# Kernel optimization log

Measured on AMD Instinct MI355X. Metric: run time of the kernel, lower is better.

Reference implementation:

```python
import jax, jax.numpy as jnp
import numpy as np

NUM_HEADS = 16
HEAD_DIM = 64
D_MODEL = NUM_HEADS * HEAD_DIM


def setup_inputs() -> dict:
    key = jax.random.key(0)
    k1, k2, k3 = jax.random.split(key, 3)
    N, T = 2, 2048
    x = jax.random.normal(k1, (N, T, D_MODEL), dtype=jnp.float32)
    mask = jnp.ones((N, T), dtype=jnp.float32)
    # fused QKV projection params (Dense: H*D*3 outputs)
    W_qkv = jax.random.normal(k2, (D_MODEL, D_MODEL * 3), dtype=jnp.float32) * (D_MODEL ** -0.5)
    b_qkv = jnp.zeros((D_MODEL * 3,), dtype=jnp.float32)
    return {"x": x, "mask": mask, "W_qkv": W_qkv, "b_qkv": b_qkv}


def reference(x, mask, W_qkv, b_qkv):
    N, T, _ = x.shape
    H, D = NUM_HEADS, HEAD_DIM
    qkv = x @ W_qkv + b_qkv                       # [N, T, H*D*3]
    qkv = qkv.reshape(N, T, H, D, 3)
    qkv = jnp.transpose(qkv, (4, 0, 2, 1, 3))     # [3, N, H, T, D]
    q, k, v = qkv[0], qkv[1], qkv[2]
    logits = jnp.einsum('bhqd,bhkd->bhqk', q, k) / (D ** 0.5)  # [N, H, T, T]
    # NOTE: original masks along the QUERY axis (broadcast over keys)
    logits = logits + (1.0 - mask)[:, None, :, None] * -1e9
    w = jax.nn.softmax(logits, axis=-1)
    out = jnp.einsum('bhqk,bhkd->bhqd', w, v)     # [N, H, T, D]
    out = jnp.transpose(out, (0, 2, 1, 3)).reshape(N, T, H * D)
    return out
```

## Files before the change

kernel.cpp:

```cpp
#include <hip/hip_runtime.h>
#include <hip/hip_bf16.h>
#include <stdint.h>

#define NHEADS 16
#define HDIM   64
#define DMODEL 1024
#define SEQ    2048
#define NB     2
#define MTOT   (NB*SEQ)
#define NTOT   (3*DMODEL)
#define KTOT   DMODEL

#define QSCALE 0.18033688011112042f

typedef __attribute__((ext_vector_type(8)))  short          bf16x8;
typedef __attribute__((ext_vector_type(4)))  float          f32x4;
typedef __attribute__((ext_vector_type(8)))  unsigned short u16x8;

__device__ __forceinline__ unsigned short f2bf(float f) {
  unsigned u = __builtin_bit_cast(unsigned, f);
  u += 0x7fffu + ((u >> 16) & 1u);
  return (unsigned short)(u >> 16);
}

__device__ __forceinline__ f32x4 vmax4(f32x4 a, f32x4 b) {
  f32x4 r;
  r[0]=fmaxf(a[0],b[0]); r[1]=fmaxf(a[1],b[1]);
  r[2]=fmaxf(a[2],b[2]); r[3]=fmaxf(a[3],b[3]);
  return r;
}

__device__ __forceinline__ void async_copy16(void* lds, const void* g) {
  __builtin_amdgcn_global_load_lds(
      (const __attribute__((address_space(1))) unsigned int*)g,
      (__attribute__((address_space(3))) unsigned int*)lds, 16, 0, 0);
}

__global__ void convert_x_kernel(const float* __restrict__ x,
                                 unsigned short* __restrict__ xb) {
  int i = blockIdx.x * 256 + threadIdx.x;
  const f32x4* xv = reinterpret_cast<const f32x4*>(x);
  f32x4 a = xv[2*i];
  f32x4 b = xv[2*i + 1];
  u16x8 r;
  r[0]=f2bf(a[0]); r[1]=f2bf(a[1]); r[2]=f2bf(a[2]); r[3]=f2bf(a[3]);
  r[4]=f2bf(b[0]); r[5]=f2bf(b[1]); r[6]=f2bf(b[2]); r[7]=f2bf(b[3]);
  reinterpret_cast<u16x8*>(xb)[i] = r;
}

__global__ void transpose_w_kernel(const float* __restrict__ W,
                                   unsigned short* __restrict__ Wt) {
  __shared__ float tile[64][65];
  int j0 = blockIdx.x * 64;
  int k0 = blockIdx.y * 64;
  int tid = threadIdx.x;
  int lr = tid >> 6;
  int lc = tid & 63;
  #pragma unroll
  for (int i = 0; i < 16; ++i) {
    int r = i*4 + lr;
    tile[r][lc] = W[(size_t)(k0 + r)*NTOT + j0 + lc];
  }
  __syncthreads();
  #pragma unroll
  for (int i = 0; i < 16; ++i) {
    int jr = i*4 + lr;
    int j  = j0 + jr;
    int oc = (j % 3)*DMODEL + (j / 3);
    Wt[(size_t)oc*KTOT + k0 + lc] = f2bf(tile[lc][jr]);
  }
}

#define BM 128
#define BN 128
#define BK2 32
#define NBX (NTOT/BN)
#define NBY (MTOT/BM)
#define EPSTRIDE 136
__launch_bounds__(256)
__global__ void qkv_gemm_kernel(const unsigned short* __restrict__ xb,
                                const unsigned short* __restrict__ wt,
                                const float* __restrict__ bqkv,
                                unsigned short* __restrict__ Qb,
                                unsigned short* __restrict__ Kb,
                                unsigned short* __restrict__ Vt) {
  __shared__ __align__(16) unsigned char gsm[128*EPSTRIDE*2];
  unsigned short* As = (unsigned short*)gsm;
  unsigned short* Bs = (unsigned short*)(gsm + 16384);
  unsigned short* Ep = (unsigned short*)gsm;

  int tid = threadIdx.x;
  int w = tid >> 6, l = tid & 63;
  int m0 = blockIdx.y * BM;
  int n0 = blockIdx.x * BN;
  int ln = l & 15, lg = l >> 4;
  int wm = (w >> 1) * 64;
  int wn = (w & 1) * 64;

  f32x4 acc[4][4];
  const f32x4 zero4 = {0.f, 0.f, 0.f, 0.f};
  #pragma unroll
  for (int i = 0; i < 4; ++i)
    #pragma unroll
    for (int j = 0; j < 4; ++j) acc[i][j] = zero4;

  #define STAGE2(BUF, KT)                                                     \
  do {                                                                        \
    _Pragma("unroll")                                                         \
    for (int i = 0; i < 2; ++i) {                                             \
      int row  = i*64 + w*16 + (l >> 2);                                      \
      int seg  = (l & 3) ^ ((row >> 1) & 3);                                  \
      async_copy16(gsm + (BUF)*8192 + i*4096 + w*1024,                        \
                   &xb[(size_t)(m0 + row)*KTOT + (KT)*BK2 + seg*8]);          \
      async_copy16(gsm + 16384 + (BUF)*8192 + i*4096 + w*1024,                \
                   &wt[(size_t)(n0 + row)*KTOT + (KT)*BK2 + seg*8]);          \
    }                                                                         \
  } while (0)

  STAGE2(0, 0);
  asm volatile("s_waitcnt vmcnt(0)" ::: "memory");
  __syncthreads();

  for (int kt = 0; kt < KTOT/BK2; ++kt) {
    int cur = kt & 1;
    if (kt < KTOT/BK2 - 1) STAGE2(cur ^ 1, kt + 1);

    bf16x8 af[4], bfr[4];
    #pragma unroll
    for (int mi = 0; mi < 4; ++mi) {
      int ra = wm + mi*16 + ln;
      af[mi] = *reinterpret_cast<const bf16x8*>(
          &As[cur*4096 + ra*BK2 + ((lg ^ ((ra >> 1) & 3)) << 3)]);
    }
    #pragma unroll
    for (int ni = 0; ni < 4; ++ni) {
      int rb = wn + ni*16 + ln;
      bfr[ni] = *reinterpret_cast<const bf16x8*>(
          &Bs[cur*4096 + rb*BK2 + ((lg ^ ((rb >> 1) & 3)) << 3)]);
    }
    #pragma unroll
    for (int mi = 0; mi < 4; ++mi)
      #pragma unroll
      for (int ni = 0; ni < 4; ++ni)
        acc[mi][ni] = __builtin_amdgcn_mfma_f32_16x16x32_bf16(af[mi], bfr[ni], acc[mi][ni], 0, 0, 0);

    __syncthreads();
  }
  #undef STAGE2

  int r4 = lg * 4;
  if (n0 >= 2*DMODEL) {
    int hd0 = n0 - 2*DMODEL;
    #pragma unroll
    for (int mi = 0; mi < 4; ++mi) {
      #pragma unroll
      for (int ni = 0; ni < 4; ++ni) {
        int col = wn + ni*16 + ln;
        float bias = bqkv[(hd0 + col)*3 + 2];
        int rb = wm + mi*16 + r4;
        ushort4 pk4;
        pk4.x = f2bf(acc[mi][ni][0] + bias);
        pk4.y = f2bf(acc[mi][ni][1] + bias);
        pk4.z = f2bf(acc[mi][ni][2] + bias);
        pk4.w = f2bf(acc[mi][ni][3] + bias);
        *reinterpret_cast<ushort4*>(&Ep[col*EPSTRIDE + rb]) = pk4;
      }
    }
    __syncthreads();
    int n = m0 >> 11, t0 = m0 & 2047;
    #pragma unroll
    for (int pass = 0; pass < 8; ++pass) {
      int hdl = pass*16 + (tid >> 4);
      int seg = tid & 15;
      bf16x8 v = *reinterpret_cast<const bf16x8*>(&Ep[hdl*EPSTRIDE + seg*8]);
      int hd = hd0 + hdl, h = hd >> 6, d = hd & 63;
      *reinterpret_cast<bf16x8*>(
          &Vt[(((size_t)(n*NHEADS + h)*HDIM + d) << 11) + t0 + seg*8]) = v;
    }
  } else {
    #pragma unroll
    for (int mi = 0; mi < 4; ++mi) {
      #pragma unroll
      for (int ni = 0; ni < 4; ++ni) {
        int nc = n0 + wn + ni*16 + ln;
        int c  = nc >> 10;
        int hd = nc & 1023;
        int h = hd >> 6, d = hd & 63;
        float bias = bqkv[hd*3 + c];
        float qs = (c == 0) ? QSCALE : 1.0f;
        #pragma unroll
        for (int j = 0; j < 4; ++j) {
          int m = m0 + wm + mi*16 + r4 + j;
          int n = m >> 11, t = m & 2047;
          unsigned short val = f2bf((acc[mi][ni][j] + bias) * qs);
          size_t nh = (size_t)(n*NHEADS + h);
          if (c == 0) Qb[((nh*SEQ + t) << 6) + d] = val;
          else        Kb[((nh*SEQ + t) << 6) + d] = val;
        }
      }
    }
  }
}

#define PROW    88
#define POFF    49152
#define PBYTES  2816
#define OREGION 4352
__launch_bounds__(512)
__global__ void attn_kernel(const unsigned short* __restrict__ Qb,
                            const unsigned short* __restrict__ Kb,
                            const unsigned short* __restrict__ Vt,
                            float* __restrict__ out) {
  __shared__ __align__(16) unsigned char smem[POFF + 8*PBYTES];
  int tid = threadIdx.x;
  int w = tid >> 6, l = tid & 63;
  int ln = l & 15, lg = l >> 4;

  unsigned short* Pw  = (unsigned short*)(smem + POFF + w * PBYTES);
  float*          obw = (float*)         (smem + w * OREGION);

  int fid  = blockIdx.x;
  int xcd  = fid & 7, idx = fid >> 3;
  int bh   = xcd * 4 + (idx >> 4);
  int qblk = idx & 15;
  int q0   = qblk * 128 + w * 16;

  const unsigned short* Qh = Qb + (size_t)bh * SEQ * HDIM;
  const unsigned short* Kh = Kb + (size_t)bh * SEQ * HDIM;
  const unsigned short* Vh = Vt + (size_t)bh * HDIM * SEQ;

  int srow = w*8 + (l >> 3);
  int sseg = (l & 7) ^ (srow & 7);

  bf16x8 qf[2];
  #pragma unroll
  for (int dw = 0; dw < 2; ++dw)
    qf[dw] = *reinterpret_cast<const bf16x8*>(&Qh[(size_t)(q0 + ln)*HDIM + dw*32 + lg*8]);

  const f32x4 zero4 = {0.f, 0.f, 0.f, 0.f};
  f32x4 o[4];
  #pragma unroll
  for (int db = 0; db < 4; ++db) o[db] = zero4;
  f32x4 psum4 = zero4;
  float mrow = -INFINITY;

  #define STAGE(BUF, KEY0)                                                    \
  do {                                                                        \
    async_copy16(smem + (BUF)*16384 + w*1024,                                 \
                 &Kh[(size_t)((KEY0) + srow)*HDIM + sseg*8]);                 \
    async_copy16(smem + (BUF)*16384 + 8192 + w*1024,                          \
                 &Vh[(size_t)srow*SEQ + (KEY0) + sseg*8]);                    \
  } while (0)

  STAGE(0, 0);
  STAGE(1, 64);
  asm volatile("s_waitcnt vmcnt(2)" ::: "memory");
  __builtin_amdgcn_s_barrier();
  asm volatile("" ::: "memory");

  int xorE = (ln & 7) << 3;
  int cur = 0, nxt2 = 2;

  for (int kv = 0; kv < 32; ++kv) {
    if (kv < 30) STAGE(nxt2, (kv + 2) * 64);

    const unsigned short* Kc = (const unsigned short*)(smem + cur*16384);
    const unsigned short* Vc = (const unsigned short*)(smem + cur*16384 + 8192);

    f32x4 s[4];
    #pragma unroll
    for (int kb = 0; kb < 4; ++kb) {
      int r = kb*16 + ln;
      bf16x8 k0 = *reinterpret_cast<const bf16x8*>(&Kc[r*HDIM + ((     lg*8) ^ xorE)]);
      bf16x8 k1 = *reinterpret_cast<const bf16x8*>(&Kc[r*HDIM + ((32 + lg*8) ^ xorE)]);
      f32x4 t0 = __builtin_amdgcn_mfma_f32_16x16x32_bf16(k0, qf[0], zero4, 0, 0, 0);
      s[kb]    = __builtin_amdgcn_mfma_f32_16x16x32_bf16(k1, qf[1], t0,    0, 0, 0);
    }

    f32x4 m4 = vmax4(vmax4(s[0], s[1]), vmax4(s[2], s[3]));
    float localmax = fmaxf(fmaxf(m4[0], m4[1]), fmaxf(m4[2], m4[3]));

    if (!__all(localmax <= mrow + 8.f)) {
      float pm = localmax;
      pm = fmaxf(pm, __shfl_xor(pm, 16));
      pm = fmaxf(pm, __shfl_xor(pm, 32));
      float mn  = fmaxf(mrow, pm);
      float scl = __builtin_amdgcn_exp2f(mrow - mn);
      mrow = mn;
      psum4 *= scl;
      #pragma unroll
      for (int db = 0; db < 4; ++db)
        #pragma unroll
        for (int r = 0; r < 4; ++r) o[db][r] *= scl;
    }

    #pragma unroll
    for (int kb = 0; kb < 4; ++kb) {
      #pragma unroll
      for (int r = 0; r < 4; ++r)
        s[kb][r] = __builtin_amdgcn_exp2f(s[kb][r] - mrow);
      psum4 += s[kb];
    }

    #pragma unroll
    for (int kb = 0; kb < 4; ++kb) {
      uint2 pk;
      asm("v_cvt_pk_bf16_f32 %0, %1, %2" : "=v"(pk.x) : "v"(s[kb][0]), "v"(s[kb][1]));
      asm("v_cvt_pk_bf16_f32 %0, %1, %2" : "=v"(pk.y) : "v"(s[kb][2]), "v"(s[kb][3]));
      *reinterpret_cast<uint2*>(&Pw[ln*PROW + kb*16 + 4*lg]) = pk;
    }

    #pragma unroll
    for (int kw = 0; kw < 2; ++kw) {
      bf16x8 pb = *reinterpret_cast<const bf16x8*>(&Pw[ln*PROW + kw*32 + lg*8]);
      #pragma unroll
      for (int db = 0; db < 4; ++db) {
        int r = db*16 + ln;
        bf16x8 vfr = *reinterpret_cast<const bf16x8*>(
            &Vc[r*64 + ((kw*32 + lg*8) ^ xorE)]);
        o[db] = __builtin_amdgcn_mfma_f32_16x16x32_bf16(vfr, pb, o[db], 0, 0, 0);
      }
    }

    if (kv < 30) asm volatile("s_waitcnt vmcnt(2)" ::: "memory");
    else         asm volatile("s_waitcnt vmcnt(0)" ::: "memory");
    __builtin_amdgcn_s_barrier();
    asm volatile("" ::: "memory");

    cur  = (cur  == 2) ? 0 : cur  + 1;
    nxt2 = (nxt2 == 2) ? 0 : nxt2 + 1;
  }
  #undef STAGE

  float ls = (psum4[0] + psum4[1]) + (psum4[2] + psum4[3]);
  ls += __shfl_xor(ls, 16);
  ls += __shfl_xor(ls, 32);
  float inv = 1.f / ls;

  #pragma unroll
  for (int db = 0; db < 4; ++db)
    #pragma unroll
    for (int r = 0; r < 4; ++r)
      obw[ln*68 + db*16 + 4*lg + r] = o[db][r] * inv;
  asm volatile("s_waitcnt lgkmcnt(0)" ::: "memory");
  int n = bh >> 4, h = bh & 15;
  #pragma unroll
  for (int p = 0; p < 4; ++p) {
    int q = p*4 + lg;
    f32x4 vv = *reinterpret_cast<const f32x4*>(&obw[q*68 + ln*4]);
    *reinterpret_cast<f32x4*>(
        &out[((size_t)(n*SEQ + q0 + q))*DMODEL + h*HDIM + ln*4]) = vv;
  }
}

extern "C" void kernel_launch(void* const* d_in, const int* in_sizes, int n_in,
                              void* d_out, int out_size, void* d_ws, size_t ws_size,
                              hipStream_t stream) {
  const float* x    = (const float*)d_in[0];
  const float* Wq   = (const float*)d_in[2];
  const float* bq   = (const float*)d_in[3];
  float* out = (float*)d_out;

  unsigned short* xb = (unsigned short*)d_ws;
  unsigned short* wt = xb + (size_t)MTOT*KTOT;
  unsigned short* Qb = wt + (size_t)NTOT*KTOT;
  unsigned short* Kb = Qb + (size_t)NB*NHEADS*SEQ*HDIM;
  unsigned short* Vt = Kb + (size_t)NB*NHEADS*SEQ*HDIM;

  convert_x_kernel<<<(MTOT*KTOT/8)/256, 256, 0, stream>>>(x, xb);
  transpose_w_kernel<<<dim3(NTOT/64, KTOT/64), 256, 0, stream>>>(Wq, wt);
  qkv_gemm_kernel<<<dim3(NBX, NBY), 256, 0, stream>>>(xb, wt, bq, Qb, Kb, Vt);
  attn_kernel<<<512, 512, 0, stream>>>(Qb, Kb, Vt, out);
}
```

Before: 107.4 us.

## Triple-buffer QKV GEMM, double-buffer attention with setprio, merge prep kernels

The x conversion and W transpose kernels are merged into one launch to save a kernel launch and tail. The QKV GEMM moves from a two-stage to a three-stage async LDS pipeline with vmcnt-based waits, so global loads can run further ahead of the MFMAs. The attention kernel goes the other way, from three LDS stages to two with a plain barrier. This frees LDS, together with a smaller P row pitch, which should allow more resident blocks per CU. It also precomputes the swizzled K/V addresses and raises wave priority around the MFMA bursts. The trade-off is less prefetch depth in attention, plus one redundant tile load on the last iteration.

```diff
diff --git a/kernel.cpp b/kernel.cpp
--- a/kernel.cpp
+++ b/kernel.cpp
@@ -36,38 +36,44 @@
       (__attribute__((address_space(3))) unsigned int*)lds, 16, 0, 0);
 }
 
-__global__ void convert_x_kernel(const float* __restrict__ x,
-                                 unsigned short* __restrict__ xb) {
-  int i = blockIdx.x * 256 + threadIdx.x;
-  const f32x4* xv = reinterpret_cast<const f32x4*>(x);
-  f32x4 a = xv[2*i];
-  f32x4 b = xv[2*i + 1];
-  u16x8 r;
-  r[0]=f2bf(a[0]); r[1]=f2bf(a[1]); r[2]=f2bf(a[2]); r[3]=f2bf(a[3]);
-  r[4]=f2bf(b[0]); r[5]=f2bf(b[1]); r[6]=f2bf(b[2]); r[7]=f2bf(b[3]);
-  reinterpret_cast<u16x8*>(xb)[i] = r;
-}
-
-__global__ void transpose_w_kernel(const float* __restrict__ W,
-                                   unsigned short* __restrict__ Wt) {
+#define CVT_BLOCKS 2048
+#define TW_BX 48
+__launch_bounds__(256)
+__global__ void prep_kernel(const float* __restrict__ x,
+                            const float* __restrict__ W,
+                            unsigned short* __restrict__ xb,
+                            unsigned short* __restrict__ Wt) {
   __shared__ float tile[64][65];
-  int j0 = blockIdx.x * 64;
-  int k0 = blockIdx.y * 64;
-  int tid = threadIdx.x;
-  int lr = tid >> 6;
-  int lc = tid & 63;
-  #pragma unroll
-  for (int i = 0; i < 16; ++i) {
-    int r = i*4 + lr;
-    tile[r][lc] = W[(size_t)(k0 + r)*NTOT + j0 + lc];
-  }
-  __syncthreads();
-  #pragma unroll
-  for (int i = 0; i < 16; ++i) {
-    int jr = i*4 + lr;
-    int j  = j0 + jr;
-    int oc = (j % 3)*DMODEL + (j / 3);
-    Wt[(size_t)oc*KTOT + k0 + lc] = f2bf(tile[lc][jr]);
+  int b = blockIdx.x;
+  if (b < CVT_BLOCKS) {
+    int i = b * 256 + threadIdx.x;
+    const f32x4* xv = reinterpret_cast<const f32x4*>(x);
+    f32x4 a = xv[2*i];
+    f32x4 c = xv[2*i + 1];
+    u16x8 r;
+    r[0]=f2bf(a[0]); r[1]=f2bf(a[1]); r[2]=f2bf(a[2]); r[3]=f2bf(a[3]);
+    r[4]=f2bf(c[0]); r[5]=f2bf(c[1]); r[6]=f2bf(c[2]); r[7]=f2bf(c[3]);
+    reinterpret_cast<u16x8*>(xb)[i] = r;
+  } else {
+    int id = b - CVT_BLOCKS;
+    int j0 = (id % TW_BX) * 64;
+    int k0 = (id / TW_BX) * 64;
+    int tid = threadIdx.x;
+    int lr = tid >> 6;
+    int lc = tid & 63;
+    #pragma unroll
+    for (int i = 0; i < 16; ++i) {
+      int r = i*4 + lr;
+      tile[r][lc] = W[(size_t)(k0 + r)*NTOT + j0 + lc];
+    }
+    __syncthreads();
+    #pragma unroll
+    for (int i = 0; i < 16; ++i) {
+      int jr = i*4 + lr;
+      int j  = j0 + jr;
+      int oc = (j % 3)*DMODEL + (j / 3);
+      Wt[(size_t)oc*KTOT + k0 + lc] = f2bf(tile[lc][jr]);
+    }
   }
 }
 
@@ -84,9 +90,9 @@
                                 unsigned short* __restrict__ Qb,
                                 unsigned short* __restrict__ Kb,
                                 unsigned short* __restrict__ Vt) {
-  __shared__ __align__(16) unsigned char gsm[128*EPSTRIDE*2];
+  __shared__ __align__(16) unsigned char gsm[49152];
   unsigned short* As = (unsigned short*)gsm;
-  unsigned short* Bs = (unsigned short*)(gsm + 16384);
+  unsigned short* Bs = (unsigned short*)(gsm + 24576);
   unsigned short* Ep = (unsigned short*)gsm;
 
   int tid = threadIdx.x;
@@ -112,18 +118,20 @@
       int seg  = (l & 3) ^ ((row >> 1) & 3);                                  \
       async_copy16(gsm + (BUF)*8192 + i*4096 + w*1024,                        \
                    &xb[(size_t)(m0 + row)*KTOT + (KT)*BK2 + seg*8]);          \
-      async_copy16(gsm + 16384 + (BUF)*8192 + i*4096 + w*1024,                \
+      async_copy16(gsm + 24576 + (BUF)*8192 + i*4096 + w*1024,                \
                    &wt[(size_t)(n0 + row)*KTOT + (KT)*BK2 + seg*8]);          \
     }                                                                         \
   } while (0)
 
   STAGE2(0, 0);
-  asm volatile("s_waitcnt vmcnt(0)" ::: "memory");
-  __syncthreads();
-
+  STAGE2(1, 1);
+  asm volatile("s_waitcnt vmcnt(4)" ::: "memory");
+  __builtin_amdgcn_s_barrier();
+  asm volatile("" ::: "memory");
+
+  int cur = 0, nxt2 = 2;
   for (int kt = 0; kt < KTOT/BK2; ++kt) {
-    int cur = kt & 1;
-    if (kt < KTOT/BK2 - 1) STAGE2(cur ^ 1, kt + 1);
+    if (kt < KTOT/BK2 - 2) STAGE2(nxt2, kt + 2);
 
     bf16x8 af[4], bfr[4];
     #pragma unroll
@@ -144,7 +152,13 @@
       for (int ni = 0; ni < 4; ++ni)
         acc[mi][ni] = __builtin_amdgcn_mfma_f32_16x16x32_bf16(af[mi], bfr[ni], acc[mi][ni], 0, 0, 0);
 
-    __syncthreads();
+    if (kt < KTOT/BK2 - 2) asm volatile("s_waitcnt vmcnt(4)" ::: "memory");
+    else                   asm volatile("s_waitcnt vmcnt(0)" ::: "memory");
+    __builtin_amdgcn_s_barrier();
+    asm volatile("" ::: "memory");
+
+    cur  = (cur  == 2) ? 0 : cur  + 1;
+    nxt2 = (nxt2 == 2) ? 0 : nxt2 + 1;
   }
   #undef STAGE2
 
@@ -202,9 +216,9 @@
   }
 }
 
-#define PROW    88
-#define POFF    49152
-#define PBYTES  2816
+#define PROW    80
+#define POFF    32768
+#define PBYTES  2560
 #define OREGION 4352
 __launch_bounds__(512)
 __global__ void attn_kernel(const unsigned short* __restrict__ Qb,
@@ -244,6 +258,13 @@
   f32x4 psum4 = zero4;
   float mrow = -INFINITY;
 
+  int xorE = (ln & 7) << 3;
+  int coff0 = (((     lg*8) ^ xorE)) * 2;
+  int coff1 = (((32 + lg*8) ^ xorE)) * 2;
+  int rbyte = ln * 128;
+  const unsigned char* kv0 = smem + rbyte + coff0;
+  const unsigned char* kv1 = smem + rbyte + coff1;
+
   #define STAGE(BUF, KEY0)                                                    \
   do {                                                                        \
     async_copy16(smem + (BUF)*16384 + w*1024,                                 \
@@ -253,32 +274,26 @@
   } while (0)
 
   STAGE(0, 0);
-  STAGE(1, 64);
-  asm volatile("s_waitcnt vmcnt(2)" ::: "memory");
-  __builtin_amdgcn_s_barrier();
-  asm volatile("" ::: "memory");
-
-  int xorE = (ln & 7) << 3;
-  int cur = 0, nxt2 = 2;
+  __syncthreads();
 
   for (int kv = 0; kv < 32; ++kv) {
-    if (kv < 30) STAGE(nxt2, (kv + 2) * 64);
-
-    const unsigned short* Kc = (const unsigned short*)(smem + cur*16384);
-    const unsigned short* Vc = (const unsigned short*)(smem + cur*16384 + 8192);
+    int cur  = kv & 1;
+    int nkey = (kv < 31) ? (kv + 1) * 64 : kv * 64;
+    STAGE(cur ^ 1, nkey);
 
     f32x4 s[4];
+    __builtin_amdgcn_s_setprio(1);
     #pragma unroll
     for (int kb = 0; kb < 4; ++kb) {
-      int r = kb*16 + ln;
-      bf16x8 k0 = *reinterpret_cast<const bf16x8*>(&Kc[r*HDIM + ((     lg*8) ^ xorE)]);
-      bf16x8 k1 = *reinterpret_cast<const bf16x8*>(&Kc[r*HDIM + ((32 + lg*8) ^ xorE)]);
+      bf16x8 k0 = *reinterpret_cast<const bf16x8*>(kv0 + cur*16384 + kb*2048);
+      bf16x8 k1 = *reinterpret_cast<const bf16x8*>(kv1 + cur*16384 + kb*2048);
       f32x4 t0 = __builtin_amdgcn_mfma_f32_16x16x32_bf16(k0, qf[0], zero4, 0, 0, 0);
       s[kb]    = __builtin_amdgcn_mfma_f32_16x16x32_bf16(k1, qf[1], t0,    0, 0, 0);
     }
+    __builtin_amdgcn_s_setprio(0);
 
     f32x4 m4 = vmax4(vmax4(s[0], s[1]), vmax4(s[2], s[3]));
-    float localmax = fmaxf(fmaxf(m4[0], m4[1]), fmaxf(m4[2], m4[3]));
+    float localmax = fmaxf(fmaxf(fmaxf(m4[0], m4[1]), m4[2]), m4[3]);
 
     if (!__all(localmax <= mrow + 8.f)) {
       float pm = localmax;
@@ -313,22 +328,18 @@
     #pragma unroll
     for (int kw = 0; kw < 2; ++kw) {
       bf16x8 pb = *reinterpret_cast<const bf16x8*>(&Pw[ln*PROW + kw*32 + lg*8]);
+      const unsigned char* vb = (kw == 0) ? kv0 : kv1;
+      __builtin_amdgcn_s_setprio(1);
       #pragma unroll
       for (int db = 0; db < 4; ++db) {
-        int r = db*16 + ln;
         bf16x8 vfr = *reinterpret_cast<const bf16x8*>(
-            &Vc[r*64 + ((kw*32 + lg*8) ^ xorE)]);
+            vb + cur*16384 + 8192 + db*2048);
         o[db] = __builtin_amdgcn_mfma_f32_16x16x32_bf16(vfr, pb, o[db], 0, 0, 0);
       }
-    }
-
-    if (kv < 30) asm volatile("s_waitcnt vmcnt(2)" ::: "memory");
-    else         asm volatile("s_waitcnt vmcnt(0)" ::: "memory");
-    __builtin_amdgcn_s_barrier();
-    asm volatile("" ::: "memory");
-
-    cur  = (cur  == 2) ? 0 : cur  + 1;
-    nxt2 = (nxt2 == 2) ? 0 : nxt2 + 1;
+      __builtin_amdgcn_s_setprio(0);
+    }
+
+    __syncthreads();
   }
   #undef STAGE
 
@@ -367,8 +378,7 @@
   unsigned short* Kb = Qb + (size_t)NB*NHEADS*SEQ*HDIM;
   unsigned short* Vt = Kb + (size_t)NB*NHEADS*SEQ*HDIM;
 
-  convert_x_kernel<<<(MTOT*KTOT/8)/256, 256, 0, stream>>>(x, xb);
-  transpose_w_kernel<<<dim3(NTOT/64, KTOT/64), 256, 0, stream>>>(Wq, wt);
+  prep_kernel<<<CVT_BLOCKS + TW_BX*(KTOT/64), 256, 0, stream>>>(x, Wq, xb, wt);
   qkv_gemm_kernel<<<dim3(NBX, NBY), 256, 0, stream>>>(xb, wt, bq, Qb, Kb, Vt);
   attn_kernel<<<512, 512, 0, stream>>>(Qb, Kb, Vt, out);
 }
```

After: 99.72 us. 1.08x faster.
